# Performance work log

Hardware: AMD Instinct MI355X
Metric: run time of the kernel (lower is better)

The kernel has to match this reference:

```python
import jax, jax.numpy as jnp
import numpy as np

N, T, H, L, E, F, CN, CG = 20000, 2, 128, 4, 320000, 514, 3, 2
EPS = 1e-7  # GENConv message epsilon


def _ln(x, g, b):
    mu = jnp.mean(x, axis=-1, keepdims=True)
    var = jnp.mean((x - mu) ** 2, axis=-1, keepdims=True)
    return (x - mu) / jnp.sqrt(var + 1e-5) * g + b


def _genconv(x, src, dst, e, W1, b1, g1, be1, W2, b2, t, n):
    # message: relu(x_j + edge_attr) + eps
    msg = jax.nn.relu(x[src] + e) + EPS  # [E,H]
    # softmax aggregation with learnable temperature t, grouped by dst
    logits = msg * t
    m = jax.ops.segment_max(logits, dst, num_segments=n)
    m = jnp.where(jnp.isfinite(m), m, 0.0)  # guard empty segments
    ex = jnp.exp(logits - m[dst])
    denom = jax.ops.segment_sum(ex, dst, num_segments=n)
    alpha = ex / (denom[dst] + 1e-16)
    agg = jax.ops.segment_sum(msg * alpha, dst, num_segments=n)  # [N,H]
    out = agg + x  # residual with root node (x_r)
    # MLP: Lin(H,2H) -> LayerNorm -> ReLU -> Lin(2H,H)
    h1 = jax.nn.relu(_ln(out @ W1 + b1, g1, be1))
    return h1 @ W2 + b2


def _attn(x, Wq, Wk, Wv, gamma):
    # x: [N, T, H]; channel (transform-axis) self-attention, gamma-gated residual
    q = jnp.einsum('tc,nch->nth', Wq, x)
    k = jnp.einsum('tc,nch->nth', Wk, x)
    v = jnp.einsum('tc,nch->nth', Wv, x)
    a = jax.nn.softmax(jnp.einsum('nth,nsh->nts', q, k), axis=-1)
    o = jnp.einsum('nts,nsh->nth', a, v)
    return gamma * o + x


def setup_inputs() -> dict:
    key = jax.random.key(0)
    ks = iter(jax.random.split(key, 48))

    def nrm(sh, s=0.02):
        return jax.random.normal(next(ks), sh, dtype=jnp.float32) * s

    inp = {}
    inp['node_feature'] = jax.random.normal(next(ks), (N, F), dtype=jnp.float32)
    inp['edge_index'] = jax.random.randint(next(ks), (T, 2, E), 0, N, dtype=jnp.int32)
    inp['edge_attr'] = jax.random.normal(next(ks), (T, E, 2), dtype=jnp.float32)
    # encoders
    inp['Wne'] = nrm((F, H)); inp['bne'] = jnp.zeros((H,), jnp.float32)
    inp['Wee'] = nrm((2, H)); inp['bee'] = jnp.zeros((H,), jnp.float32)
    # per-layer GENConv MLP params (stacked over L)
    inp['W1'] = nrm((L, H, 2 * H)); inp['b1'] = jnp.zeros((L, 2 * H), jnp.float32)
    inp['g1'] = jnp.ones((L, 2 * H), jnp.float32); inp['be1'] = jnp.zeros((L, 2 * H), jnp.float32)
    inp['W2'] = nrm((L, 2 * H, H)); inp['b2'] = jnp.zeros((L, H), jnp.float32)
    # DeepGCNLayer LayerNorms
    inp['dg'] = jnp.ones((L, H), jnp.float32); inp['db'] = jnp.zeros((L, H), jnp.float32)
    # learnable temperatures
    inp['t'] = jnp.ones((L,), jnp.float32)
    # node attention + head
    inp['Wq_n'] = nrm((T, T), 0.2); inp['Wk_n'] = nrm((T, T), 0.2); inp['Wv_n'] = nrm((T, T), 0.2)
    inp['gamma_n'] = jnp.float32(0.5)
    inp['Wn1'] = nrm((T * H, T * H)); inp['bn1'] = jnp.zeros((T * H,), jnp.float32)
    inp['Wn2'] = nrm((T * H, CN)); inp['bn2'] = jnp.zeros((CN,), jnp.float32)
    # graph attention + head
    inp['Wq_g'] = nrm((T, T), 0.2); inp['Wk_g'] = nrm((T, T), 0.2); inp['Wv_g'] = nrm((T, T), 0.2)
    inp['gamma_g'] = jnp.float32(0.5)
    inp['Wg1'] = nrm((T * H, T * H)); inp['bg1'] = jnp.zeros((T * H,), jnp.float32)
    inp['Wg2'] = nrm((T * H, CG)); inp['bg2'] = jnp.zeros((CG,), jnp.float32)
    return inp


def reference(node_feature, edge_index, edge_attr, Wne, bne, Wee, bee,
              W1, b1, g1, be1, W2, b2, dg, db, t,
              Wq_n, Wk_n, Wv_n, gamma_n, Wn1, bn1, Wn2, bn2,
              Wq_g, Wk_g, Wv_g, gamma_g, Wg1, bg1, Wg2, bg2):
    embs = []
    for ti in range(T):
        x = node_feature @ Wne + bne           # node_encoder
        e = edge_attr[ti] @ Wee + bee          # edge_encoder
        src, dst = edge_index[ti, 0], edge_index[ti, 1]
        # layers[0].conv applied directly
        x = _genconv(x, src, dst, e, W1[0], b1[0], g1[0], be1[0], W2[0], b2[0], t[0], N)
        # res+ DeepGCN blocks
        for l in range(1, L):
            h = jax.nn.relu(_ln(x, dg[l], db[l]))  # dropout p=0.1 is identity in eval
            x = x + _genconv(h, src, dst, e, W1[l], b1[l], g1[l], be1[l], W2[l], b2[l], t[l], N)
        x = jax.nn.relu(_ln(x, dg[0], db[0]))
        embs.append(x)
    emb = jnp.stack(embs, axis=1)  # [N, T, H]

    a = _attn(emb, Wq_n, Wk_n, Wv_n, gamma_n).reshape(N, T * H)
    node = jax.nn.relu(a @ Wn1 + bn1) @ Wn2 + bn2
    node = jax.nn.log_softmax(node, axis=-1)

    g = _attn(emb, Wq_g, Wk_g, Wv_g, gamma_g).reshape(N, T * H)
    gp = jnp.mean(g, axis=0, keepdims=True)  # global_mean_pool (single graph)
    gp = jax.nn.relu(gp @ Wg1 + bg1) @ Wg2 + bg2
    gp = jax.nn.log_softmax(gp, axis=-1)
    return (node, gp)
```

## Files before the change

kernel.cpp:

```cpp
#include <hip/hip_runtime.h>

#define NN 20000
#define TT 2
#define HH 128
#define LL 4
#define EE 320000
#define FF 514
#define CN 3
#define CG 2
#define MP 20096

typedef __bf16 bf16x8 __attribute__((ext_vector_type(8)));
typedef __bf16 bf16x4 __attribute__((ext_vector_type(4)));
typedef __bf16 bf16x2 __attribute__((ext_vector_type(2)));
typedef float f32x4 __attribute__((ext_vector_type(4)));

struct __align__(8) Edge { int src; __bf16 ea0, ea1; };

__device__ inline float wave_sum(float v) {
#pragma unroll
  for (int off = 32; off; off >>= 1) v += __shfl_xor(v, off);
  return v;
}
__device__ inline float red16(float v) {
  v += __shfl_xor(v, 1); v += __shfl_xor(v, 2);
  v += __shfl_xor(v, 4); v += __shfl_xor(v, 8);
  return v;
}

__device__ __forceinline__ float fexp2(float x) {
#if __has_builtin(__builtin_amdgcn_exp2f)
  return __builtin_amdgcn_exp2f(x);
#else
  return exp2f(x);
#endif
}

__device__ __forceinline__ void gload_lds16(const void* g, void* l) {
  __builtin_amdgcn_global_load_lds(
      (const __attribute__((address_space(1))) unsigned int*)g,
      (__attribute__((address_space(3))) unsigned int*)l, 16, 0, 0);
}

#define ENCB (MP / 64)
#define SCB 2500
#define CHUNK 5000
__global__ __launch_bounds__(256) void enc_scatter_kernel(
    const __bf16* __restrict__ A, const __bf16* __restrict__ BT,
    const float* __restrict__ bias, __bf16* __restrict__ C,
    const int* __restrict__ edge_index, const float* __restrict__ edge_attr,
    int* __restrict__ cursor, Edge* __restrict__ edges) {
  __shared__ __bf16 As[2][64][32];
  __shared__ __bf16 Bs[2][128][32];
  const int tid = threadIdx.x;
  if (blockIdx.x >= ENCB) {
    int chunk = blockIdx.x & 7;
    int i = ((blockIdx.x - ENCB) >> 3) * 256 + tid;
    if (i >= 2 * EE) return;
    int ti = (i >= EE) ? 1 : 0;
    int e = i - ti * EE;
    const int* srcp = edge_index + (size_t)ti * 2 * EE;
    int d = srcp[EE + e];
    int gnode = ti * NN + d;
    if (gnode / CHUNK != chunk) return;
    int s = srcp[e];
    float2 ea = ((const float2*)edge_attr)[(size_t)ti * EE + e];
    int pos = atomicAdd(&cursor[gnode], 1);
    Edge ed;
    ed.src = s + ti * MP;
    ed.ea0 = (__bf16)ea.x; ed.ea1 = (__bf16)ea.y;
    __builtin_memcpy(&edges[pos], &ed, sizeof(Edge));
    return;
  }
  const int K = 576;
  const int lane = tid & 63, w = tid >> 6;
  const int bm = blockIdx.x * 64;
  const int wr = (w >> 1) * 32, wc = (w & 1) * 64;
  const int fr = lane & 15, fq = lane >> 4;
  const int rowA = tid >> 2, chA = (tid & 3) * 8;
  const __bf16* Ab = A + (size_t)(bm + rowA) * K + chA;
  const __bf16* Bb = BT + (size_t)rowA * K + chA;
  const __bf16* Bb2 = Bb + (size_t)64 * K;
  f32x4 acc[2][4] = {};
#define STAGE(buf, k0)                                  \
  do {                                                  \
    gload_lds16(Ab + (k0), &As[buf][rowA][chA]);        \
    gload_lds16(Bb + (k0), &Bs[buf][rowA][chA]);        \
    gload_lds16(Bb2 + (k0), &Bs[buf][rowA + 64][chA]);  \
  } while (0)
  STAGE(0, 0);
  __syncthreads();
  int cur = 0;
  for (int k0 = 0; k0 < K; k0 += 32) {
    if (k0 + 32 < K) STAGE(cur ^ 1, k0 + 32);
    bf16x8 af[2], bq[4];
#pragma unroll
    for (int m = 0; m < 2; ++m)
      af[m] = *(const bf16x8*)&As[cur][wr + m * 16 + fr][fq * 8];
#pragma unroll
    for (int n = 0; n < 4; ++n)
      bq[n] = *(const bf16x8*)&Bs[cur][wc + n * 16 + fr][fq * 8];
#pragma unroll
    for (int m = 0; m < 2; ++m)
#pragma unroll
      for (int n = 0; n < 4; ++n)
        acc[m][n] =
            __builtin_amdgcn_mfma_f32_16x16x32_bf16(af[m], bq[n], acc[m][n], 0, 0, 0);
    __syncthreads();
    cur ^= 1;
  }
#undef STAGE
#pragma unroll
  for (int m = 0; m < 2; ++m) {
#pragma unroll
    for (int n = 0; n < 4; ++n) {
#pragma unroll
      for (int j = 0; j < 4; ++j) {
        int gm = bm + wr + m * 16 + fq * 4 + j;
        int gn = wc + n * 16 + fr;
        if (gm < NN) {
          __bf16 c = (__bf16)(acc[m][n][j] + bias[gn]);
          C[(size_t)gm * 128 + gn] = c;
          C[(size_t)(gm + MP) * 128 + gn] = c;
        }
      }
    }
  }
}

template <int EPI>
__global__ __launch_bounds__(256) void gemm256(
    const __bf16* __restrict__ A, const __bf16* __restrict__ BT,
    const float* __restrict__ bias, const float* __restrict__ g,
    const float* __restrict__ be, const float* __restrict__ W2h,
    const float* __restrict__ b2h, void* __restrict__ outp, int M, int K) {
  __shared__ __bf16 As[2][64][32];
  __shared__ __bf16 Bs[2][256][32];
  const int tid = threadIdx.x;
  const int lane = tid & 63, w = tid >> 6;
  const int bm = blockIdx.x * 64;
  const int wr = w * 16;
  const int fr = lane & 15, fq = lane >> 4;
  const int rowA = tid >> 2, chA = (tid & 3) * 8;
  const __bf16* Ab = A + (size_t)(bm + rowA) * K + chA;
  const __bf16* Bb = BT + (size_t)rowA * K + chA;
  f32x4 acc[16] = {};

#define STG(buf, k0)                                                \
  do {                                                              \
    gload_lds16(Ab + (k0), &As[buf][rowA][chA]);                    \
    _Pragma("unroll") for (int r = 0; r < 4; ++r)                   \
        gload_lds16(Bb + (size_t)(r * 64) * K + (k0),               \
                    &Bs[buf][rowA + r * 64][chA]);                  \
  } while (0)

  STG(0, 0);
  __syncthreads();
  int cur = 0;
  for (int k0 = 0; k0 < K; k0 += 32) {
    if (k0 + 32 < K) STG(cur ^ 1, k0 + 32);
    bf16x8 af = *(const bf16x8*)&As[cur][wr + fr][fq * 8];
#pragma unroll
    for (int n = 0; n < 16; ++n) {
      bf16x8 bq = *(const bf16x8*)&Bs[cur][n * 16 + fr][fq * 8];
      acc[n] = __builtin_amdgcn_mfma_f32_16x16x32_bf16(af, bq, acc[n], 0, 0, 0);
    }
    __syncthreads();
    cur ^= 1;
  }
#undef STG

  float cb[16];
#pragma unroll
  for (int n = 0; n < 16; ++n) cb[n] = bias[n * 16 + fr];

  if constexpr (EPI == 0) {
    float gv[16], bev[16];
#pragma unroll
    for (int n = 0; n < 16; ++n) {
      gv[n] = g[n * 16 + fr];
      bev[n] = be[n * 16 + fr];
    }
    __bf16* outb = (__bf16*)outp;
#pragma unroll
    for (int j = 0; j < 4; ++j) {
      float cj[16], s = 0.f, s2 = 0.f;
#pragma unroll
      for (int n = 0; n < 16; ++n) {
        float c = acc[n][j] + cb[n];
        cj[n] = c; s += c; s2 += c * c;
      }
      s = red16(s); s2 = red16(s2);
      float mu = s * (1.f / 256);
      float var = fmaxf(s2 * (1.f / 256) - mu * mu, 0.f);
      float rr = rsqrtf(var + 1e-5f);
      int gm = bm + wr + fq * 4 + j;
      __bf16* op = outb + (size_t)gm * 256;
#pragma unroll
      for (int n = 0; n < 16; ++n) {
        float y = (cj[n] - mu) * rr * gv[n] + bev[n];
        op[n * 16 + fr] = (__bf16)fmaxf(y, 0.f);
      }
    }
  } else {
    float w0[16], w1[16], w2[16];
#pragma unroll
    for (int n = 0; n < 16; ++n) {
      int col = n * 16 + fr;
      w0[n] = W2h[col * 3 + 0];
      w1[n] = W2h[col * 3 + 1];
      w2[n] = W2h[col * 3 + 2];
    }
    float* outf = (float*)outp;
#pragma unroll
    for (int j = 0; j < 4; ++j) {
      float p0 = 0.f, p1 = 0.f, p2 = 0.f;
#pragma unroll
      for (int n = 0; n < 16; ++n) {
        float h = fmaxf(acc[n][j] + cb[n], 0.f);
        p0 += h * w0[n]; p1 += h * w1[n]; p2 += h * w2[n];
      }
      p0 = red16(p0); p1 = red16(p1); p2 = red16(p2);
      int gm = bm + wr + fq * 4 + j;
      if (fr == 0 && gm < M) {
        float l0 = p0 + b2h[0], l1 = p1 + b2h[1], l2 = p2 + b2h[2];
        float m = fmaxf(l0, fmaxf(l1, l2));
        float lse = m + logf(__expf(l0 - m) + __expf(l1 - m) + __expf(l2 - m));
        outf[(size_t)gm * 3 + 0] = l0 - lse;
        outf[(size_t)gm * 3 + 1] = l1 - lse;
        outf[(size_t)gm * 3 + 2] = l2 - lse;
      }
    }
  }
}

template <int MODE>
__global__ __launch_bounds__(256) void gemm_lin2(
    const __bf16* __restrict__ A, const __bf16* __restrict__ BT,
    const float* __restrict__ bias, float* __restrict__ xres,
    const float* __restrict__ g, const float* __restrict__ be,
    void* __restrict__ lnout) {
  __shared__ __bf16 As[2][64][32];
  __shared__ __bf16 Bs[2][128][32];
  __shared__ float redS[64][2], redS2[64][2];
  const int tid = threadIdx.x;
  const int lane = tid & 63, w = tid >> 6;
  const int bm = blockIdx.x * 64;
  const int wr = (w >> 1) * 32, wc = (w & 1) * 64;
  const int fr = lane & 15, fq = lane >> 4;
  const int rowA = tid >> 2, chA = (tid & 3) * 8;
  const __bf16* Ab = A + (size_t)(bm + rowA) * 256 + chA;
  const __bf16* Bb = BT + (size_t)rowA * 256 + chA;
  const __bf16* Bb2 = Bb + (size_t)64 * 256;
  f32x4 acc[2][4] = {};

#define STAGE(buf, k0)                                  \
  do {                                                  \
    gload_lds16(Ab + (k0), &As[buf][rowA][chA]);        \
    gload_lds16(Bb + (k0), &Bs[buf][rowA][chA]);        \
    gload_lds16(Bb2 + (k0), &Bs[buf][rowA + 64][chA]);  \
  } while (0)

  STAGE(0, 0);
  __syncthreads();
  int cur = 0;
  for (int k0 = 0; k0 < 256; k0 += 32) {
    if (k0 + 32 < 256) STAGE(cur ^ 1, k0 + 32);
    bf16x8 af[2], bq[4];
#pragma unroll
    for (int m = 0; m < 2; ++m)
      af[m] = *(const bf16x8*)&As[cur][wr + m * 16 + fr][fq * 8];
#pragma unroll
    for (int n = 0; n < 4; ++n)
      bq[n] = *(const bf16x8*)&Bs[cur][wc + n * 16 + fr][fq * 8];
#pragma unroll
    for (int m = 0; m < 2; ++m)
#pragma unroll
      for (int n = 0; n < 4; ++n)
        acc[m][n] =
            __builtin_amdgcn_mfma_f32_16x16x32_bf16(af[m], bq[n], acc[m][n], 0, 0, 0);
    __syncthreads();
    cur ^= 1;
  }
#undef STAGE

  float cv[2][4][4];
#pragma unroll
  for (int m = 0; m < 2; ++m) {
    int r0 = wr + m * 16 + fq * 4;
#pragma unroll
    for (int j = 0; j < 4; ++j) {
      int gm = bm + r0 + j;
      float s = 0.f, s2 = 0.f;
#pragma unroll
      for (int n = 0; n < 4; ++n) {
        float c = acc[m][n][j] + bias[wc + n * 16 + fr];
        if (MODE != 0) c += xres[(size_t)gm * 128 + wc + n * 16 + fr];
        cv[m][n][j] = c;
        s += c; s2 += c * c;
      }
      s = red16(s); s2 = red16(s2);
      if (fr == 0) {
        redS[r0 + j][w & 1] = s;
        redS2[r0 + j][w & 1] = s2;
      }
    }
  }
  __syncthreads();
#pragma unroll
  for (int m = 0; m < 2; ++m) {
    int r0 = wr + m * 16 + fq * 4;
#pragma unroll
    for (int j = 0; j < 4; ++j) {
      int r = r0 + j;
      int gm = bm + r;
      float S = redS[r][0] + redS[r][1];
      float S2 = redS2[r][0] + redS2[r][1];
      float mu = S * (1.f / 128);
      float var = fmaxf(S2 * (1.f / 128) - mu * mu, 0.f);
      float rr = rsqrtf(var + 1e-5f);
      if constexpr (MODE < 2) {
        float* xp = xres + (size_t)gm * 128;
        __bf16* hp = (__bf16*)lnout + (size_t)gm * 128;
#pragma unroll
        for (int n = 0; n < 4; ++n) {
          int col = wc + n * 16 + fr;
          float c = cv[m][n][j];
          xp[col] = c;
          float y = (c - mu) * rr * g[col] + be[col];
          hp[col] = (__bf16)fmaxf(y, 0.f);
        }
      } else {
        int half = gm >= MP;
        int node = gm - half * MP;
        if (node < NN) {
          float* ep = (float*)lnout + (size_t)node * 256 + half * 128;
#pragma unroll
          for (int n = 0; n < 4; ++n) {
            int col = wc + n * 16 + fr;
            float y = (cv[m][n][j] - mu) * rr * g[col] + be[col];
            ep[col] = fmaxf(y, 0.f);
          }
        }
      }
    }
  }
}

struct WtDesc { const float* src; __bf16* dst; int K, N, Kpad; };
struct WtDescs { WtDesc d[10]; };
#define NF2B 20079
#define PADB 2422
#define WTB 2880
#define CNTB 2500

__global__ void prep_kernel(const float* __restrict__ nf_src,
                            __bf16* __restrict__ nf_dst, WtDescs descs,
                            const int* __restrict__ edge_index,
                            int* __restrict__ deg, float* __restrict__ gp_sum) {
  int b = blockIdx.x, tid = threadIdx.x;
  if (b < NF2B) {
    int i = b * 256 + tid;
    if (i >= NN * FF / 2) return;
    int row = i / 257;
    int col = (i - row * 257) * 2;
    float2 v = ((const float2*)nf_src)[i];
    bf16x2 o; o[0] = (__bf16)v.x; o[1] = (__bf16)v.y;
    *(bf16x2*)(nf_dst + (size_t)row * 576 + col) = o;
  } else if (b < NF2B + PADB) {
    int i = (b - NF2B) * 256 + tid;
    if (i >= NN * 31) return;
    int row = i / 31, j = i - row * 31;
    bf16x2 z; z[0] = (__bf16)0.f; z[1] = (__bf16)0.f;
    *(bf16x2*)(nf_dst + (size_t)row * 576 + 514 + 2 * j) = z;
  } else if (b < NF2B + PADB + WTB) {
    int wb = b - NF2B - PADB;
    WtDesc de = descs.d[wb / 288];
    int idx = (wb % 288) * 256 + tid;
    if (idx >= de.N * de.Kpad) return;
    int n = idx / de.Kpad, k = idx - n * de.Kpad;
    float v = (k < de.K) ? de.src[(size_t)k * de.N + n] : 0.f;
    de.dst[idx] = (__bf16)v;
  } else if (b < NF2B + PADB + WTB + CNTB) {
    int i = (b - NF2B - PADB - WTB) * 256 + tid;
    if (i >= 2 * EE) return;
    int ti = (i >= EE) ? 1 : 0;
    int e = i - ti * EE;
    int d = edge_index[(size_t)ti * 2 * EE + EE + e];
    atomicAdd(&deg[ti * NN + d], 1);
  } else {
    gp_sum[tid] = 0.f;
  }
}

__global__ __launch_bounds__(1024) void scan2_kernel(
    const int* __restrict__ deg_all, int* __restrict__ rowptr,
    int* __restrict__ cursor) {
  const int ti = blockIdx.x;
  const int* deg = deg_all + ti * NN;
  __shared__ int sums[1024];
  int tid = threadIdx.x;
  int chunk = (NN + 1023) / 1024;
  int begin = tid * chunk, end = min(begin + chunk, NN);
  int s = 0;
  for (int i = begin; i < end; ++i) s += deg[i];
  sums[tid] = s;
  __syncthreads();
  for (int off = 1; off < 1024; off <<= 1) {
    int v = (tid >= off) ? sums[tid - off] : 0;
    __syncthreads();
    sums[tid] += v;
    __syncthreads();
  }
  int running = ti * EE + sums[tid] - s;
  for (int i = begin; i < end; ++i) {
    rowptr[ti * NN + i] = running;
    cursor[ti * NN + i] = running;
    running += deg[i];
  }
  if (tid == 0 && ti == 1) rowptr[2 * NN] = 2 * EE;
}

__global__ __launch_bounds__(256) void agg_kernel(
    const __bf16* __restrict__ xin, const int* __restrict__ rowptr,
    const Edge* __restrict__ edges, const float* __restrict__ Wee,
    const float* __restrict__ bee, const float* __restrict__ tptr, int layer,
    __bf16* __restrict__ out) {
  int wave = threadIdx.x >> 6, lane = threadIdx.x & 63;
  int b = blockIdx.x;
  int x8 = b & 7;
  int q = x8 >> 1;
  int par = x8 & 1;
  int ti = q >> 1, chh = q & 1;
  int group = (b >> 3) * 2 + par;
  int node = group * 4 + wave;
  int gnode = ti * NN + node;
  int xrow = ti * MP + node;
  float t2 = tptr[layer] * 1.4426950408889634f;
  int qq = lane >> 4, c15 = lane & 15;
  int c0 = chh * 64 + c15 * 4;
  float den[4] = {}, num[4] = {};
  int e = rowptr[gnode];
  const int e1 = rowptr[gnode + 1];

  if (t2 > 0.f) {
    float w0p[4], w1p[4], bvp[4];
#pragma unroll
    for (int i = 0; i < 4; ++i) {
      w0p[i] = Wee[c0 + i] * t2;
      w1p[i] = Wee[HH + c0 + i] * t2;
      bvp[i] = bee[c0 + i] * t2;
    }
#define MLPF(XV, ED)                                                      \
  do {                                                                    \
    float eax = (float)(ED).ea0, eay = (float)(ED).ea1;                   \
    _Pragma("unroll") for (int i = 0; i < 4; ++i) {                       \
      float te = fmaf(eax, w0p[i], fmaf(eay, w1p[i], bvp[i]));            \
      float sm = fmaxf(fmaf((float)(XV)[i], t2, te), 0.f);                \
      float ex = fexp2(sm);                                               \
      den[i] += ex; num[i] = fmaf(sm, ex, num[i]);                        \
    }                                                                     \
  } while (0)
    for (; e + 8 <= e1; e += 8) {
      Edge E0 = edges[e + qq];
      Edge E1 = edges[e + 4 + qq];
      bf16x4 x0 = *(const bf16x4*)(xin + (size_t)E0.src * HH + c0);
      bf16x4 x1 = *(const bf16x4*)(xin + (size_t)E1.src * HH + c0);
      MLPF(x0, E0);
      MLPF(x1, E1);
    }
    if (e + qq < e1) {
      Edge E0 = edges[e + qq];
      bf16x4 x0 = *(const bf16x4*)(xin + (size_t)E0.src * HH + c0);
      MLPF(x0, E0);
    }
    if (e + 4 + qq < e1) {
      Edge E0 = edges[e + 4 + qq];
      bf16x4 x0 = *(const bf16x4*)(xin + (size_t)E0.src * HH + c0);
      MLPF(x0, E0);
    }
#undef MLPF
#pragma unroll
    for (int i = 0; i < 4; ++i) {
      den[i] += __shfl_xor(den[i], 16);
      den[i] += __shfl_xor(den[i], 32);
      num[i] += __shfl_xor(num[i], 16);
      num[i] += __shfl_xor(num[i], 32);
    }
    if (qq == 0) {
      bf16x4 xr = *(const bf16x4*)(xin + (size_t)xrow * HH + c0);
      bf16x4 o;
#pragma unroll
      for (int i = 0; i < 4; ++i)
        o[i] = (__bf16)(num[i] / (t2 * (den[i] + 1e-16f)) + (float)xr[i]);
      *(bf16x4*)(out + (size_t)xrow * HH + c0) = o;
    }
  } else {
    float w0[4], w1[4], bv[4];
#pragma unroll
    for (int i = 0; i < 4; ++i) {
      w0[i] = Wee[c0 + i];
      w1[i] = Wee[HH + c0 + i];
      bv[i] = bee[c0 + i];
    }
    for (; e + qq < e1; e += 4) {
      Edge E0 = edges[e + qq];
      bf16x4 xv = *(const bf16x4*)(xin + (size_t)E0.src * HH + c0);
      float eax = (float)E0.ea0, eay = (float)E0.ea1;
#pragma unroll
      for (int i = 0; i < 4; ++i) {
        float m =
            fmaxf((float)xv[i] + eax * w0[i] + eay * w1[i] + bv[i], 0.f) + 1e-7f;
        float ex = fexp2(m * t2);
        den[i] += ex; num[i] += m * ex;
      }
    }
#pragma unroll
    for (int i = 0; i < 4; ++i) {
      den[i] += __shfl_xor(den[i], 16);
      den[i] += __shfl_xor(den[i], 32);
      num[i] += __shfl_xor(num[i], 16);
      num[i] += __shfl_xor(num[i], 32);
    }
    if (qq == 0) {
      bf16x4 xr = *(const bf16x4*)(xin + (size_t)xrow * HH + c0);
      bf16x4 o;
#pragma unroll
      for (int i = 0; i < 4; ++i)
        o[i] = (__bf16)(num[i] / (den[i] + 1e-16f) + (float)xr[i]);
      *(bf16x4*)(out + (size_t)xrow * HH + c0) = o;
    }
  }
}

__global__ __launch_bounds__(256) void attn2_kernel(
    const float* __restrict__ emb, const float* __restrict__ Wq_n,
    const float* __restrict__ Wk_n, const float* __restrict__ Wv_n,
    const float* __restrict__ gn, const float* __restrict__ Wq_g,
    const float* __restrict__ Wk_g, const float* __restrict__ Wv_g,
    const float* __restrict__ gg, __bf16* __restrict__ outn,
    float* __restrict__ partial) {
  __shared__ float gsum[4][256];
  int wave = threadIdx.x >> 6, lane = threadIdx.x & 63;
  int tid = threadIdx.x;
  int n = blockIdx.x * 4 + wave;
  int c0 = lane * 2;
  const float* base = emb + (size_t)n * (2 * HH);
  float2 x0 = *(const float2*)(base + c0);
  float2 x1 = *(const float2*)(base + HH + c0);

#define ATTN_BODY(Wq, Wk, Wv, GAM, O0A, O0B, O1A, O1B)                        \
  {                                                                           \
    float gamma = *(GAM);                                                     \
    float wq00 = Wq[0], wq01 = Wq[1], wq10 = Wq[2], wq11 = Wq[3];             \
    float wk00 = Wk[0], wk01 = Wk[1], wk10 = Wk[2], wk11 = Wk[3];             \
    float wv00 = Wv[0], wv01 = Wv[1], wv10 = Wv[2], wv11 = Wv[3];             \
    float q0a = wq00 * x0.x + wq01 * x1.x, q0b = wq00 * x0.y + wq01 * x1.y;   \
    float q1a = wq10 * x0.x + wq11 * x1.x, q1b = wq10 * x0.y + wq11 * x1.y;   \
    float k0a = wk00 * x0.x + wk01 * x1.x, k0b = wk00 * x0.y + wk01 * x1.y;   \
    float k1a = wk10 * x0.x + wk11 * x1.x, k1b = wk10 * x0.y + wk11 * x1.y;   \
    float v0a = wv00 * x0.x + wv01 * x1.x, v0b = wv00 * x0.y + wv01 * x1.y;   \
    float v1a = wv10 * x0.x + wv11 * x1.x, v1b = wv10 * x0.y + wv11 * x1.y;   \
    float s00 = wave_sum(q0a * k0a + q0b * k0b);                              \
    float s01 = wave_sum(q0a * k1a + q0b * k1b);                              \
    float s10 = wave_sum(q1a * k0a + q1b * k0b);                              \
    float s11 = wave_sum(q1a * k1a + q1b * k1b);                              \
    float m0 = fmaxf(s00, s01);                                               \
    float e00 = __expf(s00 - m0), e01 = __expf(s01 - m0);                     \
    float i0 = 1.f / (e00 + e01);                                             \
    float a00 = e00 * i0, a01 = e01 * i0;                                     \
    float m1 = fmaxf(s10, s11);                                               \
    float e10 = __expf(s10 - m1), e11 = __expf(s11 - m1);                     \
    float i1 = 1.f / (e10 + e11);                                             \
    float a10 = e10 * i1, a11 = e11 * i1;                                     \
    O0A = gamma * (a00 * v0a + a01 * v1a) + x0.x;                             \
    O0B = gamma * (a00 * v0b + a01 * v1b) + x0.y;                             \
    O1A = gamma * (a10 * v0a + a11 * v1a) + x1.x;                             \
    O1B = gamma * (a10 * v0b + a11 * v1b) + x1.y;                             \
  }

  float n0a, n0b, n1a, n1b;
  ATTN_BODY(Wq_n, Wk_n, Wv_n, gn, n0a, n0b, n1a, n1b);
  __bf16* opn = outn + (size_t)n * (2 * HH);
  bf16x2 t0; t0[0] = (__bf16)n0a; t0[1] = (__bf16)n0b;
  bf16x2 t1; t1[0] = (__bf16)n1a; t1[1] = (__bf16)n1b;
  *(bf16x2*)(opn + c0) = t0;
  *(bf16x2*)(opn + HH + c0) = t1;

  float g0a, g0b, g1a, g1b;
  ATTN_BODY(Wq_g, Wk_g, Wv_g, gg, g0a, g0b, g1a, g1b);
  gsum[wave][c0] = g0a;
  gsum[wave][c0 + 1] = g0b;
  gsum[wave][128 + c0] = g1a;
  gsum[wave][129 + c0] = g1b;
  __syncthreads();
  partial[(size_t)blockIdx.x * 256 + tid] =
      gsum[0][tid] + gsum[1][tid] + gsum[2][tid] + gsum[3][tid];
#undef ATTN_BODY
}

__global__ __launch_bounds__(256) void pool_kernel(const float* __restrict__ partial,
                                                   float* __restrict__ gp_sum,
                                                   int nRows) {
  int c = threadIdx.x;
  float s = 0.f;
  for (int r = blockIdx.x; r < nRows; r += gridDim.x)
    s += partial[(size_t)r * 256 + c];
  atomicAdd(&gp_sum[c], s);
}

__global__ __launch_bounds__(256) void graph_head_kernel(
    const float* __restrict__ gp_sum, const float* __restrict__ Wg1,
    const float* __restrict__ bg1, const float* __restrict__ Wg2,
    const float* __restrict__ bg2, float* __restrict__ outp, float invN) {
  __shared__ float gp[256];
  __shared__ float h1[256];
  __shared__ float lg[2];
  int tid = threadIdx.x;
  gp[tid] = gp_sum[tid] * invN;
  __syncthreads();
  float acc = bg1[tid];
  for (int k = 0; k < 256; ++k) acc += gp[k] * Wg1[k * 256 + tid];
  h1[tid] = fmaxf(acc, 0.f);
  __syncthreads();
  if (tid < 2) {
    float l = bg2[tid];
    for (int c = 0; c < 256; ++c) l += h1[c] * Wg2[c * 2 + tid];
    lg[tid] = l;
  }
  __syncthreads();
  if (tid == 0) {
    float m = fmaxf(lg[0], lg[1]);
    float lse = m + logf(__expf(lg[0] - m) + __expf(lg[1] - m));
    outp[0] = lg[0] - lse;
    outp[1] = lg[1] - lse;
  }
}

extern "C" void kernel_launch(void* const* d_in, const int* in_sizes, int n_in,
                              void* d_out, int out_size, void* d_ws, size_t ws_size,
                              hipStream_t stream) {
  (void)in_sizes; (void)n_in; (void)out_size; (void)ws_size;
  const float* node_feature = (const float*)d_in[0];
  const int* edge_index = (const int*)d_in[1];
  const float* edge_attr = (const float*)d_in[2];
  const float* Wne = (const float*)d_in[3];
  const float* bne = (const float*)d_in[4];
  const float* Wee = (const float*)d_in[5];
  const float* bee = (const float*)d_in[6];
  const float* W1 = (const float*)d_in[7];
  const float* b1 = (const float*)d_in[8];
  const float* g1 = (const float*)d_in[9];
  const float* be1 = (const float*)d_in[10];
  const float* W2 = (const float*)d_in[11];
  const float* b2 = (const float*)d_in[12];
  const float* dg = (const float*)d_in[13];
  const float* db = (const float*)d_in[14];
  const float* tpar = (const float*)d_in[15];
  const float* Wq_n = (const float*)d_in[16];
  const float* Wk_n = (const float*)d_in[17];
  const float* Wv_n = (const float*)d_in[18];
  const float* gamma_n = (const float*)d_in[19];
  const float* Wn1 = (const float*)d_in[20];
  const float* bn1 = (const float*)d_in[21];
  const float* Wn2 = (const float*)d_in[22];
  const float* bn2 = (const float*)d_in[23];
  const float* Wq_g = (const float*)d_in[24];
  const float* Wk_g = (const float*)d_in[25];
  const float* Wv_g = (const float*)d_in[26];
  const float* gamma_g = (const float*)d_in[27];
  const float* Wg1 = (const float*)d_in[28];
  const float* bg1 = (const float*)d_in[29];
  const float* Wg2 = (const float*)d_in[30];
  const float* bg2 = (const float*)d_in[31];
  float* out = (float*)d_out;

  char* pc = (char*)d_ws;
  auto alloc = [&](size_t bytes) {
    char* r = pc;
    pc += (bytes + 255) & ~(size_t)255;
    return r;
  };
  float* xbuf = (float*)alloc((size_t)2 * MP * HH * 4);
  __bf16* hbuf_b = (__bf16*)alloc((size_t)2 * MP * HH * 2);
  __bf16* t256_b = (__bf16*)alloc((size_t)2 * MP * 256 * 2);
  float* emb = (float*)alloc((size_t)NN * 2 * HH * 4);
  __bf16* aggout_b = (__bf16*)alloc((size_t)2 * MP * HH * 2);
  __bf16* nf_b = (__bf16*)emb;
  __bf16* attnb = t256_b;
  float* partial = xbuf;
  __bf16* wt_ne = (__bf16*)alloc((size_t)128 * 576 * 2);
  __bf16* wt1 = (__bf16*)alloc((size_t)4 * 256 * 128 * 2);
  __bf16* wt2 = (__bf16*)alloc((size_t)4 * 128 * 256 * 2);
  __bf16* wtn1 = (__bf16*)alloc((size_t)256 * 256 * 2);
  float* gp_sum = (float*)alloc(256 * 4);
  int* deg = (int*)alloc((size_t)2 * NN * 4);
  int* cursor = (int*)alloc((size_t)2 * NN * 4);
  int* rowptr = (int*)alloc((size_t)(2 * NN + 2) * 4);
  Edge* edges = (Edge*)alloc((size_t)2 * EE * 8);

  const int gRows2 = 2 * MP / 64;

  WtDescs wd;
  wd.d[0] = {Wne, wt_ne, FF, HH, 576};
  for (int l = 0; l < 4; ++l)
    wd.d[1 + l] = {W1 + (size_t)l * HH * 256, wt1 + (size_t)l * 256 * HH, HH, 256, HH};
  for (int l = 0; l < 4; ++l)
    wd.d[5 + l] = {W2 + (size_t)l * 256 * HH, wt2 + (size_t)l * HH * 256, 256, HH, 256};
  wd.d[9] = {Wn1, wtn1, 256, 256, 256};

  hipMemsetAsync(deg, 0, 2 * NN * sizeof(int), stream);
  prep_kernel<<<NF2B + PADB + WTB + CNTB + 1, 256, 0, stream>>>(
      node_feature, nf_b, wd, edge_index, deg, gp_sum);
  scan2_kernel<<<2, 1024, 0, stream>>>(deg, rowptr, cursor);
  enc_scatter_kernel<<<ENCB + 8 * SCB, 256, 0, stream>>>(
      nf_b, wt_ne, bne, hbuf_b, edge_index, edge_attr, cursor, edges);

  for (int l = 0; l < LL; ++l) {
    agg_kernel<<<2500 * 8, 256, 0, stream>>>(hbuf_b, rowptr, edges, Wee, bee, tpar,
                                             l, aggout_b);
    gemm256<0><<<gRows2, 256, 0, stream>>>(aggout_b, wt1 + (size_t)l * 256 * HH,
                                           b1 + l * 2 * HH, g1 + l * 2 * HH,
                                           be1 + l * 2 * HH, nullptr, nullptr, t256_b,
                                           2 * MP, HH);
    const __bf16* w2l = wt2 + (size_t)l * HH * 256;
    const float* b2l = b2 + l * HH;
    if (l == 0)
      gemm_lin2<0><<<gRows2, 256, 0, stream>>>(t256_b, w2l, b2l, xbuf, dg + 1 * HH,
                                               db + 1 * HH, hbuf_b);
    else if (l < LL - 1)
      gemm_lin2<1><<<gRows2, 256, 0, stream>>>(t256_b, w2l, b2l, xbuf,
                                               dg + (l + 1) * HH, db + (l + 1) * HH,
                                               hbuf_b);
    else
      gemm_lin2<2><<<gRows2, 256, 0, stream>>>(t256_b, w2l, b2l, xbuf, dg, db, emb);
  }

  attn2_kernel<<<NN / 4, 256, 0, stream>>>(emb, Wq_n, Wk_n, Wv_n, gamma_n, Wq_g,
                                           Wk_g, Wv_g, gamma_g, attnb, partial);
  gemm256<1><<<MP / 64, 256, 0, stream>>>(attnb, wtn1, bn1, nullptr, nullptr, Wn2,
                                          bn2, out, NN, 256);
  pool_kernel<<<128, 256, 0, stream>>>(partial, gp_sum, NN / 4);
  graph_head_kernel<<<1, 256, 0, stream>>>(gp_sum, Wg1, bg1, Wg2, bg2,
                                           out + (size_t)NN * CN, 1.0f / NN);
}
```

Measured before the change: 488.4 us.

## Map one destination node per 16-lane quarter-wave in aggregation kernel

The softmax aggregation kernel now assigns each quarter-wave its own destination node instead of splitting one node's edges across four quarters. Each quarter walks its node's edge list serially, which removes the cross-quarter shuffle reductions and the masked write, and the grid shrinks by four. The cost is that lanes within a wave diverge when neighbouring nodes have different degrees, and each quarter has less memory parallelism per node.

```diff
diff --git a/kernel.cpp b/kernel.cpp
--- a/kernel.cpp
+++ b/kernel.cpp
@@ -433,11 +433,11 @@
   int par = x8 & 1;
   int ti = q >> 1, chh = q & 1;
   int group = (b >> 3) * 2 + par;
-  int node = group * 4 + wave;
+  int qq = lane >> 4, c15 = lane & 15;
+  int node = group * 16 + wave * 4 + qq;
   int gnode = ti * NN + node;
   int xrow = ti * MP + node;
   float t2 = tptr[layer] * 1.4426950408889634f;
-  int qq = lane >> 4, c15 = lane & 15;
   int c0 = chh * 64 + c15 * 4;
   float den[4] = {}, num[4] = {};
   int e = rowptr[gnode];
@@ -461,40 +461,26 @@
       den[i] += ex; num[i] = fmaf(sm, ex, num[i]);                        \
     }                                                                     \
   } while (0)
-    for (; e + 8 <= e1; e += 8) {
-      Edge E0 = edges[e + qq];
-      Edge E1 = edges[e + 4 + qq];
+    for (; e + 2 <= e1; e += 2) {
+      Edge E0 = edges[e];
+      Edge E1 = edges[e + 1];
       bf16x4 x0 = *(const bf16x4*)(xin + (size_t)E0.src * HH + c0);
       bf16x4 x1 = *(const bf16x4*)(xin + (size_t)E1.src * HH + c0);
       MLPF(x0, E0);
       MLPF(x1, E1);
     }
-    if (e + qq < e1) {
-      Edge E0 = edges[e + qq];
+    if (e < e1) {
+      Edge E0 = edges[e];
       bf16x4 x0 = *(const bf16x4*)(xin + (size_t)E0.src * HH + c0);
       MLPF(x0, E0);
     }
-    if (e + 4 + qq < e1) {
-      Edge E0 = edges[e + 4 + qq];
-      bf16x4 x0 = *(const bf16x4*)(xin + (size_t)E0.src * HH + c0);
-      MLPF(x0, E0);
-    }
 #undef MLPF
-#pragma unroll
-    for (int i = 0; i < 4; ++i) {
-      den[i] += __shfl_xor(den[i], 16);
-      den[i] += __shfl_xor(den[i], 32);
-      num[i] += __shfl_xor(num[i], 16);
-      num[i] += __shfl_xor(num[i], 32);
-    }
-    if (qq == 0) {
-      bf16x4 xr = *(const bf16x4*)(xin + (size_t)xrow * HH + c0);
-      bf16x4 o;
-#pragma unroll
-      for (int i = 0; i < 4; ++i)
-        o[i] = (__bf16)(num[i] / (t2 * (den[i] + 1e-16f)) + (float)xr[i]);
-      *(bf16x4*)(out + (size_t)xrow * HH + c0) = o;
-    }
+    bf16x4 xr = *(const bf16x4*)(xin + (size_t)xrow * HH + c0);
+    bf16x4 o;
+#pragma unroll
+    for (int i = 0; i < 4; ++i)
+      o[i] = (__bf16)(num[i] / (t2 * (den[i] + 1e-16f)) + (float)xr[i]);
+    *(bf16x4*)(out + (size_t)xrow * HH + c0) = o;
   } else {
     float w0[4], w1[4], bv[4];
 #pragma unroll
@@ -503,8 +489,8 @@
       w1[i] = Wee[HH + c0 + i];
       bv[i] = bee[c0 + i];
     }
-    for (; e + qq < e1; e += 4) {
-      Edge E0 = edges[e + qq];
+    for (; e < e1; ++e) {
+      Edge E0 = edges[e];
       bf16x4 xv = *(const bf16x4*)(xin + (size_t)E0.src * HH + c0);
       float eax = (float)E0.ea0, eay = (float)E0.ea1;
 #pragma unroll
@@ -515,21 +501,12 @@
         den[i] += ex; num[i] += m * ex;
       }
     }
-#pragma unroll
-    for (int i = 0; i < 4; ++i) {
-      den[i] += __shfl_xor(den[i], 16);
-      den[i] += __shfl_xor(den[i], 32);
-      num[i] += __shfl_xor(num[i], 16);
-      num[i] += __shfl_xor(num[i], 32);
-    }
-    if (qq == 0) {
-      bf16x4 xr = *(const bf16x4*)(xin + (size_t)xrow * HH + c0);
-      bf16x4 o;
-#pragma unroll
-      for (int i = 0; i < 4; ++i)
-        o[i] = (__bf16)(num[i] / (den[i] + 1e-16f) + (float)xr[i]);
-      *(bf16x4*)(out + (size_t)xrow * HH + c0) = o;
-    }
+    bf16x4 xr = *(const bf16x4*)(xin + (size_t)xrow * HH + c0);
+    bf16x4 o;
+#pragma unroll
+    for (int i = 0; i < 4; ++i)
+      o[i] = (__bf16)(num[i] / (den[i] + 1e-16f) + (float)xr[i]);
+    *(bf16x4*)(out + (size_t)xrow * HH + c0) = o;
   }
 }
 
@@ -717,8 +694,8 @@
       nf_b, wt_ne, bne, hbuf_b, edge_index, edge_attr, cursor, edges);
 
   for (int l = 0; l < LL; ++l) {
-    agg_kernel<<<2500 * 8, 256, 0, stream>>>(hbuf_b, rowptr, edges, Wee, bee, tpar,
-                                             l, aggout_b);
+    agg_kernel<<<625 * 8, 256, 0, stream>>>(hbuf_b, rowptr, edges, Wee, bee, tpar,
+                                            l, aggout_b);
     gemm256<0><<<gRows2, 256, 0, stream>>>(aggout_b, wt1 + (size_t)l * 256 * HH,
                                            b1 + l * 2 * HH, g1 + l * 2 * HH,
                                            be1 + l * 2 * HH, nullptr, nullptr, t256_b,
```

After: 443.6 us. 1.1x faster.
